# Performance work log

Hardware: AMD Instinct MI355X
Metric: run time of the kernel (lower is better)

Reference implementation:

```python
import jax, jax.numpy as jnp
import numpy as np

DM, H, DK = 768, 12, 64

def setup_inputs() -> dict:
    key = jax.random.key(0)
    ks = jax.random.split(key, 12)
    B, S = 6, 1024
    sc = 1.0 / np.sqrt(DM)
    return {
        "Q": jax.random.normal(ks[0], (B, S, DM), jnp.float32),
        "K": jax.random.normal(ks[1], (B, S, DM), jnp.float32),
        "V": jax.random.normal(ks[2], (B, S, DM), jnp.float32),
        "attn_mask": jax.random.randint(ks[3], (B, S, S), 0, 2) > 0,
        "W_q": jax.random.uniform(ks[4], (DM, H * DK), jnp.float32, -sc, sc),
        "b_q": jax.random.uniform(ks[5], (H * DK,), jnp.float32, -sc, sc),
        "W_k": jax.random.uniform(ks[6], (DM, H * DK), jnp.float32, -sc, sc),
        "b_k": jax.random.uniform(ks[7], (H * DK,), jnp.float32, -sc, sc),
        "W_v": jax.random.uniform(ks[8], (DM, H * DK), jnp.float32, -sc, sc),
        "b_v": jax.random.uniform(ks[9], (H * DK,), jnp.float32, -sc, sc),
        "W_o": jax.random.uniform(ks[10], (H * DK, DM), jnp.float32, -1/np.sqrt(H*DK), 1/np.sqrt(H*DK)),
        "b_o": jax.random.uniform(ks[11], (DM,), jnp.float32, -1/np.sqrt(H*DK), 1/np.sqrt(H*DK)),
        "gamma": jnp.ones((DM,), jnp.float32),
        "beta": jnp.zeros((DM,), jnp.float32),
    }

def reference(Q, K, V, attn_mask, W_q, b_q, W_k, b_k, W_v, b_v, W_o, b_o, gamma, beta):
    B, S, _ = Q.shape
    residual = Q
    # projections -> [B, H, S, DK]
    q = (Q @ W_q + b_q).reshape(B, S, H, DK).transpose(0, 2, 1, 3)
    k = (K @ W_k + b_k).reshape(B, S, H, DK).transpose(0, 2, 1, 3)
    v = (V @ W_v + b_v).reshape(B, S, H, DK).transpose(0, 2, 1, 3)
    scores = jnp.einsum('bhqd,bhkd->bhqk', q, k) / np.sqrt(DK)
    scores = jnp.where(attn_mask[:, None, :, :], -1e9, scores)
    attn = jax.nn.softmax(scores, axis=-1)
    context = jnp.einsum('bhqk,bhkd->bhqd', attn, v)
    context = context.transpose(0, 2, 1, 3).reshape(B, S, H * DK)
    output = context @ W_o + b_o
    x = output + residual
    mu = jnp.mean(x, axis=-1, keepdims=True)
    var = jnp.var(x, axis=-1, keepdims=True)
    out = (x - mu) / jnp.sqrt(var + 1e-5) * gamma + beta
    return out, attn
```

## Files before the change

kernel.cpp:

```cpp
#include <hip/hip_runtime.h>
#include <hip/hip_bf16.h>

#define B 6
#define S 1024
#define H 12
#define DK 64
#define DM 768
#define M (B*S)
#define BH (B*H)

typedef __bf16 bf16;
typedef __attribute__((ext_vector_type(8))) __bf16 bf16x8;
typedef __attribute__((ext_vector_type(4))) float f32x4;

#define MFMA __builtin_amdgcn_mfma_f32_16x16x32_bf16

#define QSCALE 0.18033688011112042f

__device__ __forceinline__ float ex2(float x) {
  float r;
  asm("v_exp_f32 %0, %1" : "=v"(r) : "v"(x));
  return r;
}

__device__ __forceinline__ void lds_barrier() {
  asm volatile("s_waitcnt lgkmcnt(0)" ::: "memory");
  __builtin_amdgcn_s_barrier();
}

__global__ void k_prep(const float* __restrict__ Q, const float* __restrict__ K,
                       const float* __restrict__ V,
                       const float* __restrict__ Wq, const float* __restrict__ Wk,
                       const float* __restrict__ Wv, const float* __restrict__ Wo,
                       bf16* __restrict__ xb, bf16* __restrict__ wt) {
  int z = blockIdx.y;
  if (z < 3) {
    const float* X = z==0?Q : z==1?K : V;
    size_t i = ((size_t)blockIdx.x*256 + threadIdx.x)*8;
    float4 a = *(const float4*)(X + i);
    float4 b = *(const float4*)(X + i + 4);
    bf16x8 r;
    r[0]=(bf16)a.x; r[1]=(bf16)a.y; r[2]=(bf16)a.z; r[3]=(bf16)a.w;
    r[4]=(bf16)b.x; r[5]=(bf16)b.y; r[6]=(bf16)b.z; r[7]=(bf16)b.w;
    *(bf16x8*)(xb + (size_t)z*M*DM + i) = r;
  } else {
    int zz = z - 3;
    const float* W = zz==0?Wq : zz==1?Wk : zz==2?Wv : Wo;
    int idx = blockIdx.x*256 + threadIdx.x;
    int k = idx / DM, n = idx % DM;
    wt[(size_t)zz*DM*DM + (size_t)n*DM + k] = (bf16)W[idx];
  }
}


__global__ __launch_bounds__(256, 3) void k_proj(
    const bf16* __restrict__ xb, const bf16* __restrict__ wt,
    const float* __restrict__ bq, const float* __restrict__ bk,
    const float* __restrict__ bv,
    bf16* __restrict__ qb, bf16* __restrict__ kb, bf16* __restrict__ vt) {
  int z = blockIdx.z;
  const bf16* X    = xb + (size_t)z*M*DM;
  const float* bias = z==0?bq : z==1?bk : bv;
  const bf16* Wt = wt + (size_t)z*DM*DM;
  int tid = threadIdx.x, lane = tid & 63, w = tid >> 6;
  int wr = w >> 1, wc = w & 1;
  int lr = lane & 15, lg = lane >> 4;
  int m0 = blockIdx.x*128;
  int n0 = blockIdx.y*128;

  __shared__ bf16 As[2][128*32];
  __shared__ bf16 Bs[2][128*32];

  const int srow = tid >> 1;
  const int c0   = (tid & 1) * 2;
  const int f    = (srow >> 1) & 3;
  const int sc   = (c0 ^ f) & ~1;
  const bool sw  = (f & 1);
  const bf16* asrc = X  + (size_t)(m0 + srow)*DM + sc*8;
  const bf16* bsrc = Wt + (size_t)(n0 + srow)*DM + sc*8;
  const int dst0 = srow*32 + c0*8;

  const int fs = (lr >> 1) & 3;
  const int fchunk = (lg ^ fs) * 8;

  f32x4 acc[4][4];
  #pragma unroll
  for (int i=0;i<4;++i)
    #pragma unroll
    for (int j=0;j<4;++j) acc[i][j] = (f32x4){0.f,0.f,0.f,0.f};

  {
    bf16x8 a0 = *(const bf16x8*)(asrc);
    bf16x8 a1 = *(const bf16x8*)(asrc + 8);
    bf16x8 b0 = *(const bf16x8*)(bsrc);
    bf16x8 b1 = *(const bf16x8*)(bsrc + 8);
    *(bf16x8*)&As[0][dst0]     = sw ? a1 : a0;
    *(bf16x8*)&As[0][dst0 + 8] = sw ? a0 : a1;
    *(bf16x8*)&Bs[0][dst0]     = sw ? b1 : b0;
    *(bf16x8*)&Bs[0][dst0 + 8] = sw ? b0 : b1;
  }
  lds_barrier();

  for (int t = 0; t < 24; ++t) {
    int cur = t & 1;
    bf16x8 pa0, pa1, pb0, pb1;
    if (t < 23) {
      int k0 = (t+1)*32;
      pa0 = *(const bf16x8*)(asrc + k0);
      pa1 = *(const bf16x8*)(asrc + k0 + 8);
      pb0 = *(const bf16x8*)(bsrc + k0);
      pb1 = *(const bf16x8*)(bsrc + k0 + 8);
    }
    bf16x8 af[4], bfr[4];
    #pragma unroll
    for (int mi=0;mi<4;++mi) af[mi]  = *(const bf16x8*)&As[cur][(wr*64 + mi*16 + lr)*32 + fchunk];
    #pragma unroll
    for (int ni=0;ni<4;++ni) bfr[ni] = *(const bf16x8*)&Bs[cur][(wc*64 + ni*16 + lr)*32 + fchunk];
    #pragma unroll
    for (int mi=0;mi<4;++mi)
      #pragma unroll
      for (int ni=0;ni<4;++ni)
        acc[mi][ni] = MFMA(af[mi], bfr[ni], acc[mi][ni], 0,0,0);
    if (t < 23) {
      *(bf16x8*)&As[cur^1][dst0]     = sw ? pa1 : pa0;
      *(bf16x8*)&As[cur^1][dst0 + 8] = sw ? pa0 : pa1;
      *(bf16x8*)&Bs[cur^1][dst0]     = sw ? pb1 : pb0;
      *(bf16x8*)&Bs[cur^1][dst0 + 8] = sw ? pb0 : pb1;
      lds_barrier();
    }
  }

  int mw = m0 + wr*64, nw = n0 + wc*64;
  #pragma unroll
  for (int ni=0;ni<4;++ni) {
    int n = nw + ni*16 + lr;
    float bs = bias[n];
    int h = n >> 6, d = n & 63;
    #pragma unroll
    for (int mi=0;mi<4;++mi)
      #pragma unroll
      for (int r=0;r<4;++r) {
        int m = mw + mi*16 + lg*4 + r;
        int bb = m >> 10, s = m & 1023;
        float val = acc[mi][ni][r] + bs;
        if (z == 0) {
          qb[((size_t)(bb*H + h)*S + s)*DK + d] = (bf16)(val * QSCALE);
        } else if (z == 1) {
          int dsw = ((((d>>3) ^ (s&7))) << 3) | (d&7);
          kb[((size_t)(bb*H + h)*S + s)*DK + dsw] = (bf16)val;
        } else {
          int ssw = (s & ~63) | ((((s&63)>>3) ^ (d&7)) << 3) | (s&7);
          vt[((size_t)(bb*H + h)*DK + d)*S + ssw] = (bf16)val;
        }
      }
  }
}

__global__ __launch_bounds__(256, 3) void k_oproj(
    const bf16* __restrict__ ctx, const bf16* __restrict__ wto,
    const float* __restrict__ bo, const float* __restrict__ res,
    float* __restrict__ x) {
  int tid = threadIdx.x, lane = tid & 63, w = tid >> 6;
  int wr = w >> 1, wc = w & 1;
  int lr = lane & 15, lg = lane >> 4;
  int m0 = blockIdx.x*128;
  int n0 = blockIdx.y*128;

  __shared__ bf16 As[2][128*32];
  __shared__ bf16 Bs[2][128*32];

  const int srow = tid >> 1;
  const int c0   = (tid & 1) * 2;
  const int f    = (srow >> 1) & 3;
  const int sc   = (c0 ^ f) & ~1;
  const bool sw  = (f & 1);
  const bf16* asrc = ctx + (size_t)(m0 + srow)*DM + sc*8;
  const bf16* bsrc = wto + (size_t)(n0 + srow)*DM + sc*8;
  const int dst0 = srow*32 + c0*8;
  const int fs = (lr >> 1) & 3;
  const int fchunk = (lg ^ fs) * 8;

  f32x4 acc[4][4];
  #pragma unroll
  for (int i=0;i<4;++i)
    #pragma unroll
    for (int j=0;j<4;++j) acc[i][j] = (f32x4){0.f,0.f,0.f,0.f};

  {
    bf16x8 a0 = *(const bf16x8*)(asrc);
    bf16x8 a1 = *(const bf16x8*)(asrc + 8);
    bf16x8 b0 = *(const bf16x8*)(bsrc);
    bf16x8 b1 = *(const bf16x8*)(bsrc + 8);
    *(bf16x8*)&As[0][dst0]     = sw ? a1 : a0;
    *(bf16x8*)&As[0][dst0 + 8] = sw ? a0 : a1;
    *(bf16x8*)&Bs[0][dst0]     = sw ? b1 : b0;
    *(bf16x8*)&Bs[0][dst0 + 8] = sw ? b0 : b1;
  }
  lds_barrier();

  for (int t = 0; t < 24; ++t) {
    int cur = t & 1;
    bf16x8 pa0, pa1, pb0, pb1;
    if (t < 23) {
      int k0 = (t+1)*32;
      pa0 = *(const bf16x8*)(asrc + k0);
      pa1 = *(const bf16x8*)(asrc + k0 + 8);
      pb0 = *(const bf16x8*)(bsrc + k0);
      pb1 = *(const bf16x8*)(bsrc + k0 + 8);
    }
    bf16x8 af[4], bfr[4];
    #pragma unroll
    for (int mi=0;mi<4;++mi) af[mi]  = *(const bf16x8*)&As[cur][(wr*64 + mi*16 + lr)*32 + fchunk];
    #pragma unroll
    for (int ni=0;ni<4;++ni) bfr[ni] = *(const bf16x8*)&Bs[cur][(wc*64 + ni*16 + lr)*32 + fchunk];
    #pragma unroll
    for (int mi=0;mi<4;++mi)
      #pragma unroll
      for (int ni=0;ni<4;++ni)
        acc[mi][ni] = MFMA(af[mi], bfr[ni], acc[mi][ni], 0,0,0);
    if (t < 23) {
      *(bf16x8*)&As[cur^1][dst0]     = sw ? pa1 : pa0;
      *(bf16x8*)&As[cur^1][dst0 + 8] = sw ? pa0 : pa1;
      *(bf16x8*)&Bs[cur^1][dst0]     = sw ? pb1 : pb0;
      *(bf16x8*)&Bs[cur^1][dst0 + 8] = sw ? pb0 : pb1;
      lds_barrier();
    }
  }

  int mw = m0 + wr*64, nw = n0 + wc*64;
  #pragma unroll
  for (int ni=0;ni<4;++ni) {
    int n = nw + ni*16 + lr;
    float bb = bo[n];
    #pragma unroll
    for (int mi=0;mi<4;++mi)
      #pragma unroll
      for (int r=0;r<4;++r) {
        int m = mw + mi*16 + lg*4 + r;
        x[(size_t)m*DM + n] = acc[mi][ni][r] + bb + res[(size_t)m*DM + n];
      }
  }
}

__device__ __forceinline__ unsigned pk2(float a, float b) {
  union { bf16 h[2]; unsigned u; } x;
  x.h[0] = (bf16)a; x.h[1] = (bf16)b;
  return x.u;
}

__global__ __launch_bounds__(256, 4) void k_fattn(
    const bf16* __restrict__ qb, const bf16* __restrict__ kb,
    const bf16* __restrict__ vt, const unsigned char* __restrict__ mask,
    float* __restrict__ attn, bf16* __restrict__ ctx) {
  int lin = blockIdx.x + 16*blockIdx.y;
  int xcd  = lin & 7;
  int slot = lin >> 3;
  int qt   = slot & 15;
  int bh   = xcd*9 + (slot >> 4);
  int b = bh / H, h = bh - b*H;
  int tid = threadIdx.x, lane = tid & 63, w = tid >> 6;
  int lr = lane & 15, lg = lane >> 4;
  int q0 = qt*64 + w*16;

  __shared__ bf16 Kb[2][4096];
  __shared__ bf16 Vb[2][4096];
  __shared__ bf16 pt[4][2][512];

  const bf16* qbase = qb + ((size_t)bh*S + q0 + lr)*DK + lg*8;
  bf16x8 qa0 = *(const bf16x8*)(qbase);
  bf16x8 qa1 = *(const bf16x8*)(qbase + 32);

  const char* kg = (const char*)(kb + (size_t)bh*S*DK);
  const char* vg = (const char*)(vt + (size_t)bh*DK*S);
  const unsigned char* mrow = mask + ((size_t)b*S + q0 + lr)*S;
  float* abase = attn + ((size_t)bh*S + q0 + lr)*S;

  const int koff0 = w*2048 + lane*16, koff1 = koff0 + 1024;
  const int kd0 = w*1024 + lane*8,    kd1 = kd0 + 512;
  const int vrow0 = w*16 + (lane>>3), vrow1 = vrow0 + 8;
  const int vcb = (lane&7)*16;
  const int vd0 = vrow0*64 + (lane&7)*8, vd1 = vd0 + 512;

  const int krow = lr*64;
  const int kf0o = krow + ((lg ^ (lr&7))<<3);
  const int kf1o = krow + (((4+lg) ^ (lr&7))<<3);
  const int swz  = (lr & 3) << 4;

  {
    bf16x8 a0 = *(const bf16x8*)(kg + koff0);
    bf16x8 a1 = *(const bf16x8*)(kg + koff1);
    *(bf16x8*)&Kb[0][kd0] = a0;
    *(bf16x8*)&Kb[0][kd1] = a1;
  }
  uchar4 mkn[4];
  #pragma unroll
  for (int i=0;i<4;++i) mkn[i] = *(const uchar4*)(mrow + i*16 + lg*4);
  lds_barrier();

  float sum = 0.f;
  for (int t = 0; t < 16; ++t) {
    int cur = t & 1;
    uchar4 mkc[4];
    #pragma unroll
    for (int i=0;i<4;++i) mkc[i] = mkn[i];
    bf16x8 kn0, kn1;
    if (t < 15) {
      kn0 = *(const bf16x8*)(kg + (t+1)*8192 + koff0);
      kn1 = *(const bf16x8*)(kg + (t+1)*8192 + koff1);
      #pragma unroll
      for (int i=0;i<4;++i) mkn[i] = *(const uchar4*)(mrow + (t+1)*64 + i*16 + lg*4);
    }
    #pragma unroll
    for (int i=0;i<4;++i) {
      bf16x8 kf0 = *(const bf16x8*)&Kb[cur][i*1024 + kf0o];
      bf16x8 kf1 = *(const bf16x8*)&Kb[cur][i*1024 + kf1o];
      f32x4 sc = {0.f,0.f,0.f,0.f};
      sc = MFMA(kf0, qa0, sc, 0,0,0);
      sc = MFMA(kf1, qa1, sc, 0,0,0);
      sum += mkc[i].x ? 0.f : ex2(sc[0]);
      sum += mkc[i].y ? 0.f : ex2(sc[1]);
      sum += mkc[i].z ? 0.f : ex2(sc[2]);
      sum += mkc[i].w ? 0.f : ex2(sc[3]);
    }
    if (t < 15) {
      *(bf16x8*)&Kb[cur^1][kd0] = kn0;
      *(bf16x8*)&Kb[cur^1][kd1] = kn1;
    }
    lds_barrier();
  }
  sum += __shfl_xor(sum, 16);
  sum += __shfl_xor(sum, 32);
  float inv = 1.f / sum;

  f32x4 cacc[4];
  #pragma unroll
  for (int d=0;d<4;++d) cacc[d] = (f32x4){0.f,0.f,0.f,0.f};

  {
    bf16x8 a0 = *(const bf16x8*)(kg + koff0);
    bf16x8 a1 = *(const bf16x8*)(kg + koff1);
    bf16x8 b0 = *(const bf16x8*)(vg + (size_t)vrow0*2048 + vcb);
    bf16x8 b1 = *(const bf16x8*)(vg + (size_t)vrow1*2048 + vcb);
    *(bf16x8*)&Kb[0][kd0] = a0;
    *(bf16x8*)&Kb[0][kd1] = a1;
    *(bf16x8*)&Vb[0][vd0] = b0;
    *(bf16x8*)&Vb[0][vd1] = b1;
    #pragma unroll
    for (int i=0;i<4;++i) mkn[i] = *(const uchar4*)(mrow + i*16 + lg*4);
  }
  lds_barrier();

  for (int t = 0; t < 16; ++t) {
    int cur = t & 1;
    uchar4 mkc[4];
    #pragma unroll
    for (int i=0;i<4;++i) mkc[i] = mkn[i];
    bf16x8 kn0, kn1, vn0, vn1;
    if (t < 15) {
      kn0 = *(const bf16x8*)(kg + (t+1)*8192 + koff0);
      kn1 = *(const bf16x8*)(kg + (t+1)*8192 + koff1);
      vn0 = *(const bf16x8*)(vg + (size_t)vrow0*2048 + (t+1)*128 + vcb);
      vn1 = *(const bf16x8*)(vg + (size_t)vrow1*2048 + (t+1)*128 + vcb);
      #pragma unroll
      for (int i=0;i<4;++i) mkn[i] = *(const uchar4*)(mrow + (t+1)*64 + i*16 + lg*4);
    }
    #pragma unroll
    for (int u = 0; u < 2; ++u) {
      char* buf = (char*)&pt[w][u][0];
      #pragma unroll
      for (int half = 0; half < 2; ++half) {
        int i = u*2 + half;
        bf16x8 kf0 = *(const bf16x8*)&Kb[cur][i*1024 + kf0o];
        bf16x8 kf1 = *(const bf16x8*)&Kb[cur][i*1024 + kf1o];
        f32x4 sc = {0.f,0.f,0.f,0.f};
        sc = MFMA(kf0, qa0, sc, 0,0,0);
        sc = MFMA(kf1, qa1, sc, 0,0,0);
        float p0 = mkc[i].x ? 0.f : ex2(sc[0])*inv;
        float p1 = mkc[i].y ? 0.f : ex2(sc[1])*inv;
        float p2 = mkc[i].z ? 0.f : ex2(sc[2])*inv;
        float p3 = mkc[i].w ? 0.f : ex2(sc[3])*inv;
        *(float4*)(abase + t*64 + i*16 + lg*4) = (float4){p0,p1,p2,p3};
        uint2 pw2; pw2.x = pk2(p0,p1); pw2.y = pk2(p2,p3);
        *(uint2*)(buf + lr*64 + ((half*32 + lg*8) ^ swz)) = pw2;
      }
      bf16x8 pa = *(const bf16x8*)(buf + lr*64 + ((lg*16) ^ swz));
      #pragma unroll
      for (int dd=0; dd<4; ++dd) {
        bf16x8 vf = *(const bf16x8*)&Vb[cur][dd*1024 + lr*64 + ((((u*4+lg) ^ (lr&7)))<<3)];
        cacc[dd] = MFMA(pa, vf, cacc[dd], 0,0,0);
      }
    }
    if (t < 15) {
      *(bf16x8*)&Kb[cur^1][kd0] = kn0;
      *(bf16x8*)&Kb[cur^1][kd1] = kn1;
      *(bf16x8*)&Vb[cur^1][vd0] = vn0;
      *(bf16x8*)&Vb[cur^1][vd1] = vn1;
    }
    lds_barrier();
  }

  #pragma unroll
  for (int d=0;d<4;++d)
    #pragma unroll
    for (int r=0;r<4;++r)
      ctx[((size_t)b*S + q0 + lg*4 + r)*DM + h*DK + d*16 + lr] = (bf16)cacc[d][r];
}

__global__ void k_ln(const float* __restrict__ x, const float* __restrict__ gamma,
                     const float* __restrict__ beta, float* __restrict__ out) {
  int row = blockIdx.x; int tid = threadIdx.x;
  const float* xr = x + (size_t)row*DM;
  float v0 = xr[tid], v1 = xr[tid+256], v2 = xr[tid+512];
  float s = v0+v1+v2, ss = v0*v0+v1*v1+v2*v2;
  #pragma unroll
  for (int off=32; off; off>>=1){ s += __shfl_xor(s,off); ss += __shfl_xor(ss,off); }
  __shared__ float sm[8];
  int w = tid>>6;
  if ((tid&63)==0){ sm[w]=s; sm[4+w]=ss; }
  __syncthreads();
  s = sm[0]+sm[1]+sm[2]+sm[3]; ss = sm[4]+sm[5]+sm[6]+sm[7];
  float mean = s * (1.f/DM);
  float var = ss * (1.f/DM) - mean*mean;
  float rstd = rsqrtf(var + 1e-5f);
  out[(size_t)row*DM + tid]     = (v0-mean)*rstd*gamma[tid]     + beta[tid];
  out[(size_t)row*DM + tid+256] = (v1-mean)*rstd*gamma[tid+256] + beta[tid+256];
  out[(size_t)row*DM + tid+512] = (v2-mean)*rstd*gamma[tid+512] + beta[tid+512];
}

extern "C" void kernel_launch(void* const* d_in, const int* in_sizes, int n_in,
                              void* d_out, int out_size, void* d_ws, size_t ws_size,
                              hipStream_t stream) {
  const float* Q  = (const float*)d_in[0];
  const float* K  = (const float*)d_in[1];
  const float* V  = (const float*)d_in[2];
  const unsigned char* mask = (const unsigned char*)d_in[3];
  const float* Wq = (const float*)d_in[4];
  const float* bq = (const float*)d_in[5];
  const float* Wk = (const float*)d_in[6];
  const float* bk = (const float*)d_in[7];
  const float* Wv = (const float*)d_in[8];
  const float* bv = (const float*)d_in[9];
  const float* Wo = (const float*)d_in[10];
  const float* bo = (const float*)d_in[11];
  const float* gamma = (const float*)d_in[12];
  const float* beta  = (const float*)d_in[13];

  char* ws = (char*)d_ws;
  bf16* wt  = (bf16*)(ws + 0);
  bf16* xb  = (bf16*)(ws + 4718592);
  bf16* qb  = (bf16*)(ws + 33030144);
  bf16* kb  = (bf16*)(ws + 42467328);
  bf16* vt  = (bf16*)(ws + 51904512);
  bf16* ctx = (bf16*)(ws + 61341696);
  float* x  = (float*)(ws + 4718592);

  float* out  = (float*)d_out;
  float* attn = out + (size_t)B*S*DM;

  k_prep  <<<dim3(2304,7),  256, 0, stream>>>(Q,K,V,Wq,Wk,Wv,Wo,xb,wt);
  k_proj  <<<dim3(48,6,3),  256, 0, stream>>>(xb,wt,bq,bk,bv,qb,kb,vt);
  k_fattn <<<dim3(16,BH),   256, 0, stream>>>(qb,kb,vt,mask,attn,ctx);
  k_oproj <<<dim3(48,6),    256, 0, stream>>>(ctx, wt + (size_t)3*DM*DM, bo, Q, x);
  k_ln    <<<dim3(M),       256, 0, stream>>>(x,gamma,beta,out);
}
```

Before: 247.7 us.

## Halve flash-attention key tile to 32 to cut LDS and raise occupancy

Shrinks the per-iteration K/V tile in the attention kernel from 64 to 32 keys, halving the LDS buffers. The V-transpose swizzle in the projection kernel changes to match the narrower tile. Launch bounds rise from 4 to 5 blocks per CU so more waves can hide latency. In exchange there are twice as many loop iterations and barriers, and each global load is smaller.

```diff
diff --git a/kernel.cpp b/kernel.cpp
--- a/kernel.cpp
+++ b/kernel.cpp
@@ -149,7 +149,7 @@
           int dsw = ((((d>>3) ^ (s&7))) << 3) | (d&7);
           kb[((size_t)(bb*H + h)*S + s)*DK + dsw] = (bf16)val;
         } else {
-          int ssw = (s & ~63) | ((((s&63)>>3) ^ (d&7)) << 3) | (s&7);
+          int ssw = (s & ~31) | ((((s&31)>>3) ^ ((d>>1)&3)) << 3) | (s&7);
           vt[((size_t)(bb*H + h)*DK + d)*S + ssw] = (bf16)val;
         }
       }
@@ -248,7 +248,7 @@
   return x.u;
 }
 
-__global__ __launch_bounds__(256, 4) void k_fattn(
+__global__ __launch_bounds__(256, 5) void k_fattn(
     const bf16* __restrict__ qb, const bf16* __restrict__ kb,
     const bf16* __restrict__ vt, const unsigned char* __restrict__ mask,
     float* __restrict__ attn, bf16* __restrict__ ctx) {
@@ -262,9 +262,9 @@
   int lr = lane & 15, lg = lane >> 4;
   int q0 = qt*64 + w*16;
 
-  __shared__ bf16 Kb[2][4096];
-  __shared__ bf16 Vb[2][4096];
-  __shared__ bf16 pt[4][2][512];
+  __shared__ bf16 Kb[2][2048];
+  __shared__ bf16 Vb[2][2048];
+  __shared__ bf16 pt[4][512];
 
   const bf16* qbase = qb + ((size_t)bh*S + q0 + lr)*DK + lg*8;
   bf16x8 qa0 = *(const bf16x8*)(qbase);
@@ -275,56 +275,49 @@
   const unsigned char* mrow = mask + ((size_t)b*S + q0 + lr)*S;
   float* abase = attn + ((size_t)bh*S + q0 + lr)*S;
 
-  const int koff0 = w*2048 + lane*16, koff1 = koff0 + 1024;
-  const int kd0 = w*1024 + lane*8,    kd1 = kd0 + 512;
-  const int vrow0 = w*16 + (lane>>3), vrow1 = vrow0 + 8;
-  const int vcb = (lane&7)*16;
-  const int vd0 = vrow0*64 + (lane&7)*8, vd1 = vd0 + 512;
+  const int kofB = tid*16;
+  const int kdE  = tid*8;
+  const char* vsrc = vg + (size_t)(tid>>2)*2048 + (tid&3)*16;
 
   const int krow = lr*64;
   const int kf0o = krow + ((lg ^ (lr&7))<<3);
   const int kf1o = krow + (((4+lg) ^ (lr&7))<<3);
-  const int swz  = (lr & 3) << 4;
+  const int vfo  = ((lg ^ ((lr>>1)&3)) << 3);
+  const int swzP = (lr & 3) << 4;
 
   {
-    bf16x8 a0 = *(const bf16x8*)(kg + koff0);
-    bf16x8 a1 = *(const bf16x8*)(kg + koff1);
-    *(bf16x8*)&Kb[0][kd0] = a0;
-    *(bf16x8*)&Kb[0][kd1] = a1;
-  }
-  uchar4 mkn[4];
-  #pragma unroll
-  for (int i=0;i<4;++i) mkn[i] = *(const uchar4*)(mrow + i*16 + lg*4);
+    bf16x8 a0 = *(const bf16x8*)(kg + kofB);
+    *(bf16x8*)&Kb[0][kdE] = a0;
+  }
+  uchar4 mkn0 = *(const uchar4*)(mrow + lg*4);
+  uchar4 mkn1 = *(const uchar4*)(mrow + 16 + lg*4);
   lds_barrier();
 
   float sum = 0.f;
-  for (int t = 0; t < 16; ++t) {
+  for (int t = 0; t < 32; ++t) {
     int cur = t & 1;
-    uchar4 mkc[4];
-    #pragma unroll
-    for (int i=0;i<4;++i) mkc[i] = mkn[i];
-    bf16x8 kn0, kn1;
-    if (t < 15) {
-      kn0 = *(const bf16x8*)(kg + (t+1)*8192 + koff0);
-      kn1 = *(const bf16x8*)(kg + (t+1)*8192 + koff1);
-      #pragma unroll
-      for (int i=0;i<4;++i) mkn[i] = *(const uchar4*)(mrow + (t+1)*64 + i*16 + lg*4);
-    }
-    #pragma unroll
-    for (int i=0;i<4;++i) {
+    uchar4 mkc0 = mkn0, mkc1 = mkn1;
+    bf16x8 kn0;
+    if (t < 31) {
+      kn0 = *(const bf16x8*)(kg + (t+1)*4096 + kofB);
+      mkn0 = *(const uchar4*)(mrow + (t+1)*32 + lg*4);
+      mkn1 = *(const uchar4*)(mrow + (t+1)*32 + 16 + lg*4);
+    }
+    #pragma unroll
+    for (int i=0;i<2;++i) {
       bf16x8 kf0 = *(const bf16x8*)&Kb[cur][i*1024 + kf0o];
       bf16x8 kf1 = *(const bf16x8*)&Kb[cur][i*1024 + kf1o];
       f32x4 sc = {0.f,0.f,0.f,0.f};
       sc = MFMA(kf0, qa0, sc, 0,0,0);
       sc = MFMA(kf1, qa1, sc, 0,0,0);
-      sum += mkc[i].x ? 0.f : ex2(sc[0]);
-      sum += mkc[i].y ? 0.f : ex2(sc[1]);
-      sum += mkc[i].z ? 0.f : ex2(sc[2]);
-      sum += mkc[i].w ? 0.f : ex2(sc[3]);
-    }
-    if (t < 15) {
-      *(bf16x8*)&Kb[cur^1][kd0] = kn0;
-      *(bf16x8*)&Kb[cur^1][kd1] = kn1;
+      uchar4 mkc = i ? mkc1 : mkc0;
+      sum += mkc.x ? 0.f : ex2(sc[0]);
+      sum += mkc.y ? 0.f : ex2(sc[1]);
+      sum += mkc.z ? 0.f : ex2(sc[2]);
+      sum += mkc.w ? 0.f : ex2(sc[3]);
+    }
+    if (t < 31) {
+      *(bf16x8*)&Kb[cur^1][kdE] = kn0;
     }
     lds_barrier();
   }
@@ -337,64 +330,51 @@
   for (int d=0;d<4;++d) cacc[d] = (f32x4){0.f,0.f,0.f,0.f};
 
   {
-    bf16x8 a0 = *(const bf16x8*)(kg + koff0);
-    bf16x8 a1 = *(const bf16x8*)(kg + koff1);
-    bf16x8 b0 = *(const bf16x8*)(vg + (size_t)vrow0*2048 + vcb);
-    bf16x8 b1 = *(const bf16x8*)(vg + (size_t)vrow1*2048 + vcb);
-    *(bf16x8*)&Kb[0][kd0] = a0;
-    *(bf16x8*)&Kb[0][kd1] = a1;
-    *(bf16x8*)&Vb[0][vd0] = b0;
-    *(bf16x8*)&Vb[0][vd1] = b1;
-    #pragma unroll
-    for (int i=0;i<4;++i) mkn[i] = *(const uchar4*)(mrow + i*16 + lg*4);
+    bf16x8 a0 = *(const bf16x8*)(kg + kofB);
+    bf16x8 v0 = *(const bf16x8*)(vsrc);
+    *(bf16x8*)&Kb[0][kdE] = a0;
+    *(bf16x8*)&Vb[0][kdE] = v0;
+    mkn0 = *(const uchar4*)(mrow + lg*4);
+    mkn1 = *(const uchar4*)(mrow + 16 + lg*4);
   }
   lds_barrier();
 
-  for (int t = 0; t < 16; ++t) {
+  char* buf = (char*)&pt[w][0];
+  for (int t = 0; t < 32; ++t) {
     int cur = t & 1;
-    uchar4 mkc[4];
-    #pragma unroll
-    for (int i=0;i<4;++i) mkc[i] = mkn[i];
-    bf16x8 kn0, kn1, vn0, vn1;
-    if (t < 15) {
-      kn0 = *(const bf16x8*)(kg + (t+1)*8192 + koff0);
-      kn1 = *(const bf16x8*)(kg + (t+1)*8192 + koff1);
-      vn0 = *(const bf16x8*)(vg + (size_t)vrow0*2048 + (t+1)*128 + vcb);
-      vn1 = *(const bf16x8*)(vg + (size_t)vrow1*2048 + (t+1)*128 + vcb);
-      #pragma unroll
-      for (int i=0;i<4;++i) mkn[i] = *(const uchar4*)(mrow + (t+1)*64 + i*16 + lg*4);
-    }
-    #pragma unroll
-    for (int u = 0; u < 2; ++u) {
-      char* buf = (char*)&pt[w][u][0];
-      #pragma unroll
-      for (int half = 0; half < 2; ++half) {
-        int i = u*2 + half;
-        bf16x8 kf0 = *(const bf16x8*)&Kb[cur][i*1024 + kf0o];
-        bf16x8 kf1 = *(const bf16x8*)&Kb[cur][i*1024 + kf1o];
-        f32x4 sc = {0.f,0.f,0.f,0.f};
-        sc = MFMA(kf0, qa0, sc, 0,0,0);
-        sc = MFMA(kf1, qa1, sc, 0,0,0);
-        float p0 = mkc[i].x ? 0.f : ex2(sc[0])*inv;
-        float p1 = mkc[i].y ? 0.f : ex2(sc[1])*inv;
-        float p2 = mkc[i].z ? 0.f : ex2(sc[2])*inv;
-        float p3 = mkc[i].w ? 0.f : ex2(sc[3])*inv;
-        *(float4*)(abase + t*64 + i*16 + lg*4) = (float4){p0,p1,p2,p3};
-        uint2 pw2; pw2.x = pk2(p0,p1); pw2.y = pk2(p2,p3);
-        *(uint2*)(buf + lr*64 + ((half*32 + lg*8) ^ swz)) = pw2;
-      }
-      bf16x8 pa = *(const bf16x8*)(buf + lr*64 + ((lg*16) ^ swz));
-      #pragma unroll
-      for (int dd=0; dd<4; ++dd) {
-        bf16x8 vf = *(const bf16x8*)&Vb[cur][dd*1024 + lr*64 + ((((u*4+lg) ^ (lr&7)))<<3)];
-        cacc[dd] = MFMA(pa, vf, cacc[dd], 0,0,0);
-      }
-    }
-    if (t < 15) {
-      *(bf16x8*)&Kb[cur^1][kd0] = kn0;
-      *(bf16x8*)&Kb[cur^1][kd1] = kn1;
-      *(bf16x8*)&Vb[cur^1][vd0] = vn0;
-      *(bf16x8*)&Vb[cur^1][vd1] = vn1;
+    uchar4 mkc0 = mkn0, mkc1 = mkn1;
+    bf16x8 kn0, vn0;
+    if (t < 31) {
+      kn0 = *(const bf16x8*)(kg + (t+1)*4096 + kofB);
+      vn0 = *(const bf16x8*)(vsrc + (t+1)*64);
+      mkn0 = *(const uchar4*)(mrow + (t+1)*32 + lg*4);
+      mkn1 = *(const uchar4*)(mrow + (t+1)*32 + 16 + lg*4);
+    }
+    #pragma unroll
+    for (int i=0;i<2;++i) {
+      bf16x8 kf0 = *(const bf16x8*)&Kb[cur][i*1024 + kf0o];
+      bf16x8 kf1 = *(const bf16x8*)&Kb[cur][i*1024 + kf1o];
+      f32x4 sc = {0.f,0.f,0.f,0.f};
+      sc = MFMA(kf0, qa0, sc, 0,0,0);
+      sc = MFMA(kf1, qa1, sc, 0,0,0);
+      uchar4 mkc = i ? mkc1 : mkc0;
+      float p0 = mkc.x ? 0.f : ex2(sc[0])*inv;
+      float p1 = mkc.y ? 0.f : ex2(sc[1])*inv;
+      float p2 = mkc.z ? 0.f : ex2(sc[2])*inv;
+      float p3 = mkc.w ? 0.f : ex2(sc[3])*inv;
+      *(float4*)(abase + t*32 + i*16 + lg*4) = (float4){p0,p1,p2,p3};
+      uint2 pw2; pw2.x = pk2(p0,p1); pw2.y = pk2(p2,p3);
+      *(uint2*)(buf + lr*64 + ((i*32 + lg*8) ^ swzP)) = pw2;
+    }
+    bf16x8 pa = *(const bf16x8*)(buf + lr*64 + ((lg*16) ^ swzP));
+    #pragma unroll
+    for (int dd=0; dd<4; ++dd) {
+      bf16x8 vf = *(const bf16x8*)&Vb[cur][(dd*16 + lr)*32 + vfo];
+      cacc[dd] = MFMA(pa, vf, cacc[dd], 0,0,0);
+    }
+    if (t < 31) {
+      *(bf16x8*)&Kb[cur^1][kdE] = kn0;
+      *(bf16x8*)&Vb[cur^1][kdE] = vn0;
     }
     lds_barrier();
   }
```

New measurement: 262.2 us, median of 2. +5.8%, slower.
